# Optimization experiments

Measured on AMD Instinct MI355X. Metric: run time of the kernel, lower is better.

## Reference

```python
import jax, jax.numpy as jnp
import numpy as np

N_NODES = 50000
N_EDGES = 800000
EPS = 1e-5


def setup_inputs() -> dict:
    key = jax.random.key(0)
    ks = jax.random.split(key, 8)
    x = jax.random.normal(ks[0], (N_NODES, 4), dtype=jnp.float32)
    edge_index = jax.random.randint(ks[1], (2, N_EDGES), 0, N_NODES, dtype=jnp.int64)
    edge_attr = jax.random.normal(ks[2], (N_EDGES, 84), dtype=jnp.float32)
    # nnconv1 (acts as Linear(88,128) over concatenated per-edge features)
    W1 = jax.random.normal(ks[3], (88, 128), dtype=jnp.float32) * (1.0 / np.sqrt(88))
    b1 = jnp.zeros((128,), dtype=jnp.float32)
    # BatchNorm1d(128) affine params
    gamma = jnp.ones((128,), dtype=jnp.float32)
    beta = jnp.zeros((128,), dtype=jnp.float32)
    # node_mlp_2: Linear(132,64) + ReLU
    W2 = jax.random.normal(ks[4], (132, 64), dtype=jnp.float32) * (1.0 / np.sqrt(132))
    b2 = jnp.zeros((64,), dtype=jnp.float32)
    return {"x": x, "edge_index": edge_index, "edge_attr": edge_attr,
            "W1": W1, "b1": b1, "gamma": gamma, "beta": beta, "W2": W2, "b2": b2}


def reference(x, edge_index, edge_attr, W1, b1, gamma, beta, W2, b2):
    row, col = edge_index[0], edge_index[1]
    n_nodes = x.shape[0]
    # gather + concat: [E, 4+84=88]
    h = jnp.concatenate([x[col], edge_attr], axis=1)
    # edge-conditioned linear (NNConv wrapper == Linear(88,128)): [E,128]
    h = h @ W1 + b1
    # BatchNorm1d over edge batch dim (training mode, biased var as torch)
    mean = jnp.mean(h, axis=0)
    var = jnp.mean((h - mean) ** 2, axis=0)
    h = (h - mean) * jax.lax.rsqrt(var + EPS) * gamma + beta
    # scatter_mean over row -> [N,128]
    agg = jax.ops.segment_sum(h, row, num_segments=n_nodes)
    cnt = jax.ops.segment_sum(jnp.ones((h.shape[0],), dtype=h.dtype), row,
                              num_segments=n_nodes)
    agg = agg / jnp.clip(cnt, 1.0)[:, None]
    # concat + MLP: [N, 4+128=132] -> [N,64]
    out = jnp.concatenate([x, agg], axis=1)
    return jax.nn.relu(out @ W2 + b2)
```

## Files before the change

kernel.cpp:

```cpp
#include <hip/hip_runtime.h>
#include <hip/hip_bf16.h>

#define E_EDGES 800000
#define N_NODES_ 50000
#define EPS_ 1e-5f
#define N_SCAN_BLOCKS 49

#define M_GRID   625
#define M_ITERS  10
#define M_SPLITS 25

typedef float f32x4 __attribute__((ext_vector_type(4)));
typedef short s16x8 __attribute__((ext_vector_type(8)));

#define OFF_M      0
#define OFF_CS     (88 * 88)
#define OFF_CNT    (OFF_CS + 88)
#define ZERO_WORDS (OFF_CNT + N_NODES_)
#define OFF_AGG    ZERO_WORDS
#define OFF_CUR    (OFF_AGG + N_NODES_ * 88)
#define OFF_PART   (OFF_CUR + N_NODES_)
#define OFF_PERM   (OFF_PART + 64)
#define OFF_V      (OFF_PERM + E_EDGES)
#define OFF_S      (OFF_V + 88 * 128)
#define OFF_T      (OFF_S + 128)
#define OFF_MPART  (OFF_T + 128)

__global__ __launch_bounds__(256, 3)
void m_kernel(const float* __restrict__ x, const int* __restrict__ eidx,
              const float* __restrict__ ea, float* __restrict__ mpart)
{
    __shared__ __align__(16) short Gs_t[96 * 136];

    const int tid  = threadIdx.x;
    const int lane = tid & 63;
    const int wave = tid >> 6;
    const int m    = lane & 15;
    const int q    = lane >> 4;

    f32x4 acc[6];
#pragma unroll
    for (int i = 0; i < 6; ++i) acc[i] = (f32x4){0.f, 0.f, 0.f, 0.f};

    {
        int* gz = (int*)&Gs_t[88 * 136];
        for (int i = tid; i < 8 * 136 / 2; i += 256) gz[i] = 0;
    }

    unsigned addrL[21];
#pragma unroll
    for (int i = 0; i < 21; ++i) {
        const int d = (i * 256 + tid) * 2;
        const int e = d / 84;
        const int f = d - e * 84;
        addrL[i] = (unsigned)((4 + f) * 136 + e);
    }

    int tile = blockIdx.x;
    int colA = 0, colB = 0;
    if (tid < 128) colA = eidx[E_EDGES + tile * 128 + tid];
    float2 r[21];
    {
        const float2* tb = (const float2*)ea + (size_t)tile * 5376;
#pragma unroll
        for (int i = 0; i < 21; ++i) r[i] = tb[i * 256 + tid];
    }
    float4 xv = (float4){0.f, 0.f, 0.f, 0.f};
    if (tid < 128) xv = *(const float4*)(x + (size_t)colA * 4);
    if (tid < 128) colB = eidx[E_EDGES + (tile + M_GRID) * 128 + tid];

#pragma unroll 1
    for (int it = 0; it < M_ITERS; ++it) {
        __syncthreads();

        if (tid < 128) {
            __hip_bfloat16 b0 = __float2bfloat16(xv.x);
            __hip_bfloat16 b1 = __float2bfloat16(xv.y);
            __hip_bfloat16 b2 = __float2bfloat16(xv.z);
            __hip_bfloat16 b3 = __float2bfloat16(xv.w);
            Gs_t[0 * 136 + tid] = *(short*)&b0;
            Gs_t[1 * 136 + tid] = *(short*)&b1;
            Gs_t[2 * 136 + tid] = *(short*)&b2;
            Gs_t[3 * 136 + tid] = *(short*)&b3;
        }
#pragma unroll
        for (int i = 0; i < 21; ++i) {
            __hip_bfloat16 b0 = __float2bfloat16(r[i].x);
            __hip_bfloat16 b1 = __float2bfloat16(r[i].y);
            Gs_t[addrL[i]]       = *(short*)&b0;
            Gs_t[addrL[i] + 136] = *(short*)&b1;
        }

        const int next = tile + M_GRID;
        if (it + 1 < M_ITERS) {
            const float2* tbn = (const float2*)ea + (size_t)next * 5376;
#pragma unroll
            for (int i = 0; i < 21; ++i) r[i] = tbn[i * 256 + tid];
            if (tid < 128) xv = *(const float4*)(x + (size_t)colB * 4);
            if (tid < 128 && it + 2 < M_ITERS)
                colB = eidx[E_EDGES + (next + M_GRID) * 128 + tid];
        }
        __syncthreads();

#pragma unroll
        for (int kk = 0; kk < 4; ++kk) {
            const int kbase = kk * 32 + q * 8;
            s16x8 fr[6];
#pragma unroll
            for (int p = 0; p < 6; ++p)
                fr[p] = *reinterpret_cast<const s16x8*>(
                            &Gs_t[(p * 16 + m) * 136 + kbase]);
#define MM(i, a, b) acc[i] = __builtin_amdgcn_mfma_f32_16x16x32_bf16(fr[a], fr[b], acc[i], 0, 0, 0)
            if      (wave == 0) { MM(0,0,0); MM(1,0,4); MM(2,1,3); MM(3,2,3); MM(4,3,4); MM(5,5,5); }
            else if (wave == 1) { MM(0,0,1); MM(1,0,5); MM(2,1,4); MM(3,2,4); MM(4,3,5); }
            else if (wave == 2) { MM(0,0,2); MM(1,1,1); MM(2,1,5); MM(3,2,5); MM(4,4,4); }
            else                { MM(0,0,3); MM(1,1,2); MM(2,2,2); MM(3,3,3); MM(4,4,5); }
#undef MM
        }
        tile = next;
    }

    {
        float* pb = mpart + (size_t)blockIdx.x * 5376;
        const int nt = (wave == 0) ? 6 : 5;
#pragma unroll
        for (int i = 0; i < 6; ++i) {
            if (i < nt) {
                const int k = wave + i * 4;
                *(f32x4*)(pb + k * 256 + m * 16 + q * 4) = acc[i];
            }
        }
    }
}

__global__ __launch_bounds__(256)
void m_reduce_kernel(const float* __restrict__ mpart, float* __restrict__ M)
{
    const int g     = blockIdx.x * 256 + threadIdx.x;
    const int pos   = g % 5376;
    const int split = g / 5376;
    const int b0    = split * (M_GRID / M_SPLITS);
    const int b1    = b0 + (M_GRID / M_SPLITS);

    float s = 0.f;
#pragma unroll 5
    for (int b = b0; b < b1; ++b) s += mpart[(size_t)b * 5376 + pos];

    const int k  = pos >> 8;
    const int wi = pos & 255;
    const int m  = wi >> 4;
    const int qr = wi & 15;
    const int tr = (k >= 20) ? 5 : (k >= 18) ? 4 : (k >= 15) ? 3
                 : (k >= 11) ? 2 : (k >= 6) ? 1 : 0;
    const int S  = (tr == 5) ? 20 : (tr == 4) ? 18 : (tr == 3) ? 15
                 : (tr == 2) ? 11 : (tr == 1) ? 6 : 0;
    const int tc = tr + (k - S);
    const int rr = tr * 16 + qr;
    const int c  = tc * 16 + m;
    if (rr < 88 && c < 88) {
        atomicAdd(&M[rr * 88 + c], s);
        if (tr != tc) atomicAdd(&M[c * 88 + rr], s);
    }
}

__global__ void hist_kernel(const int* __restrict__ eidx, int* __restrict__ cnt)
{
    int e = blockIdx.x * 256 + threadIdx.x;
    if (e < E_EDGES) atomicAdd(&cnt[eidx[e]], 1);
}

__global__ void scan1_kernel(const int* __restrict__ cnt, int* __restrict__ partial)
{
    __shared__ int l[1024];
    int i = blockIdx.x * 1024 + threadIdx.x;
    l[threadIdx.x] = (i < N_NODES_) ? cnt[i] : 0;
    __syncthreads();
    for (int s = 512; s > 0; s >>= 1) {
        if (threadIdx.x < s) l[threadIdx.x] += l[threadIdx.x + s];
        __syncthreads();
    }
    if (threadIdx.x == 0) partial[blockIdx.x] = l[0];
}

__global__ void scan2_kernel(int* __restrict__ partial)
{
    if (threadIdx.x == 0) {
        int acc = 0;
        for (int i = 0; i < N_SCAN_BLOCKS; ++i) {
            int t = partial[i]; partial[i] = acc; acc += t;
        }
    }
}

__global__ void scan3_kernel(const int* __restrict__ cnt, const int* __restrict__ partial,
                             int* __restrict__ cursor)
{
    __shared__ int l[1024];
    int i = blockIdx.x * 1024 + threadIdx.x;
    int v = (i < N_NODES_) ? cnt[i] : 0;
    l[threadIdx.x] = v;
    __syncthreads();
    for (int s = 1; s < 1024; s <<= 1) {
        int t = (threadIdx.x >= s) ? l[threadIdx.x - s] : 0;
        __syncthreads();
        l[threadIdx.x] += t;
        __syncthreads();
    }
    if (i < N_NODES_) cursor[i] = partial[blockIdx.x] + l[threadIdx.x] - v;
}

__global__ void scatter_kernel(const int* __restrict__ eidx, int* __restrict__ cursor,
                               int* __restrict__ perm)
{
    int e = blockIdx.x * 256 + threadIdx.x;
    if (e < E_EDGES) {
        int pos = atomicAdd(&cursor[eidx[e]], 1);
        perm[pos] = e;
    }
}

__global__ __launch_bounds__(256)
void agg_kernel(const float* __restrict__ x, const int* __restrict__ eidx,
                const float* __restrict__ ea, const int* __restrict__ perm,
                const int* __restrict__ cursor, const int* __restrict__ cnt,
                float* __restrict__ agg)
{
    __shared__ float comb[2][88];
    const int tid  = threadIdx.x;
    const int w    = tid >> 6;
    const int lane = tid & 63;
    const int nloc = w >> 1;
    const int par  = w & 1;
    const int node = blockIdx.x * 2 + nloc;

    const int end = cursor[node];
    float a0 = 0.f, a1 = 0.f;
    int i = end - cnt[node] + par;
    if (i < end) {
        int e   = perm[i];
        int col = eidx[E_EDGES + e];
        for (; i < end; i += 2) {
            const float* p = ea + (size_t)e * 84;
            float v0 = (lane < 4) ? x[(size_t)col * 4 + lane] : p[lane - 4];
            float v1 = (lane < 24) ? p[60 + lane] : 0.f;
            int e_n = 0, col_n = 0;
            if (i + 2 < end) {
                e_n   = perm[i + 2];
                col_n = eidx[E_EDGES + e_n];
            }
            a0 += v0;
            a1 += v1;
            e = e_n; col = col_n;
        }
    }
    if (par == 1) {
        comb[nloc][lane] = a0;
        if (lane < 24) comb[nloc][64 + lane] = a1;
    }
    __syncthreads();
    if (par == 0) {
        a0 += comb[nloc][lane];
        if (lane < 24) a1 += comb[nloc][64 + lane];
        agg[(size_t)node * 88 + lane] = a0;
        if (lane < 24) agg[(size_t)node * 88 + 64 + lane] = a1;
    }
}

__global__ void colsum_kernel(const float* __restrict__ agg, float* __restrict__ cs)
{
    const int f = threadIdx.x;
    if (f >= 88) return;
    float a = 0.f;
    for (int n = blockIdx.x; n < N_NODES_; n += gridDim.x) a += agg[n * 88 + f];
    atomicAdd(&cs[f], a);
}

__global__ void mv_kernel(const float* __restrict__ M, const float* __restrict__ W1,
                          float* __restrict__ v)
{
    const int a = blockIdx.x;
    const int j = threadIdx.x;
    float acc = 0.f;
    for (int b = 0; b < 88; ++b) acc += M[a * 88 + b] * W1[b * 128 + j];
    v[a * 128 + j] = acc;
}

__global__ void stats_kernel(const float* __restrict__ cs, const float* __restrict__ v,
                             const float* __restrict__ W1, const float* __restrict__ b1,
                             const float* __restrict__ gamma, const float* __restrict__ beta,
                             float* __restrict__ s, float* __restrict__ t)
{
    const int j = threadIdx.x;
    const float invE = 1.0f / (float)E_EDGES;
    float mu = 0.f, eh2 = 0.f;
    for (int a = 0; a < 88; ++a) {
        float w = W1[a * 128 + j];
        mu  += cs[a] * w;
        eh2 += v[a * 128 + j] * w;
    }
    mu *= invE;
    eh2 *= invE;
    float var  = eh2 - mu * mu;
    float mean = mu + b1[j];
    float inv  = rsqrtf(var + EPS_);
    float sj   = gamma[j] * inv;
    s[j] = sj;
    t[j] = beta[j] - mean * sj;
}

__global__ __launch_bounds__(128)
void node_kernel(const float* __restrict__ x, const float* __restrict__ agg,
                 const int* __restrict__ cnt, const float* __restrict__ W1,
                 const float* __restrict__ b1, const float* __restrict__ W2,
                 const float* __restrict__ b2, const float* __restrict__ s,
                 const float* __restrict__ t, float* __restrict__ out)
{
    __shared__ float aggL[4 * 88];
    __shared__ float featL[4][128];
    __shared__ float cntL[4];
    __shared__ float xL[16];
    const int tid = threadIdx.x;
    const int nbase = blockIdx.x * 4;

    for (int i = tid; i < 352; i += 128) aggL[i] = agg[nbase * 88 + i];
    if (tid < 4)  cntL[tid] = (float)cnt[nbase + tid];
    if (tid < 16) xL[tid] = x[nbase * 4 + tid];
    __syncthreads();

    {
        const int j = tid;
        float a0 = 0.f, a1 = 0.f, a2 = 0.f, a3 = 0.f;
        for (int a = 0; a < 88; ++a) {
            float w = W1[a * 128 + j];
            a0 += aggL[a]       * w;
            a1 += aggL[88 + a]  * w;
            a2 += aggL[176 + a] * w;
            a3 += aggL[264 + a] * w;
        }
        const float sj = s[j], tj = t[j], bj = b1[j];
        float accs[4] = {a0, a1, a2, a3};
#pragma unroll
        for (int n = 0; n < 4; ++n) {
            float c = cntL[n];
            featL[n][j] = (c > 0.f) ? (sj * (accs[n] / c + bj) + tj) : 0.f;
        }
    }
    __syncthreads();

    {
        const int jc = tid & 63;
        const int nh = tid >> 6;
#pragma unroll
        for (int h = 0; h < 2; ++h) {
            const int n = nh * 2 + h;
            float acc = b2[jc];
#pragma unroll
            for (int k = 0; k < 4; ++k) acc += xL[n * 4 + k] * W2[k * 64 + jc];
            for (int k = 0; k < 128; ++k)
                acc += featL[n][k] * W2[(4 + k) * 64 + jc];
            out[(nbase + n) * 64 + jc] = fmaxf(acc, 0.f);
        }
    }
}

extern "C" void kernel_launch(void* const* d_in, const int* in_sizes, int n_in,
                              void* d_out, int out_size, void* d_ws, size_t ws_size,
                              hipStream_t stream)
{
    const float* x     = (const float*)d_in[0];
    const int*   eidx  = (const int*)d_in[1];
    const float* ea    = (const float*)d_in[2];
    const float* W1    = (const float*)d_in[3];
    const float* b1    = (const float*)d_in[4];
    const float* gamma = (const float*)d_in[5];
    const float* beta  = (const float*)d_in[6];
    const float* W2    = (const float*)d_in[7];
    const float* b2    = (const float*)d_in[8];

    float* ws    = (float*)d_ws;
    float* M     = ws + OFF_M;
    float* cs    = ws + OFF_CS;
    int*   cnt   = (int*)(ws + OFF_CNT);
    float* agg   = ws + OFF_AGG;
    int*   cur   = (int*)(ws + OFF_CUR);
    int*   part  = (int*)(ws + OFF_PART);
    int*   perm  = (int*)(ws + OFF_PERM);
    float* v     = ws + OFF_V;
    float* s     = ws + OFF_S;
    float* t     = ws + OFF_T;
    float* mpart = ws + OFF_MPART;
    float* out   = (float*)d_out;

    hipMemsetAsync(d_ws, 0, (size_t)ZERO_WORDS * sizeof(float), stream);

    hist_kernel<<<(E_EDGES + 255) / 256, 256, 0, stream>>>(eidx, cnt);
    scan1_kernel<<<N_SCAN_BLOCKS, 1024, 0, stream>>>(cnt, part);
    scan2_kernel<<<1, 64, 0, stream>>>(part);
    scan3_kernel<<<N_SCAN_BLOCKS, 1024, 0, stream>>>(cnt, part, cur);
    scatter_kernel<<<(E_EDGES + 255) / 256, 256, 0, stream>>>(eidx, cur, perm);

    m_kernel<<<M_GRID, 256, 0, stream>>>(x, eidx, ea, mpart);
    m_reduce_kernel<<<(5376 * M_SPLITS) / 256, 256, 0, stream>>>(mpart, M);
    agg_kernel<<<N_NODES_ / 2, 256, 0, stream>>>(x, eidx, ea, perm, cur, cnt, agg);

    colsum_kernel<<<512, 96, 0, stream>>>(agg, cs);
    mv_kernel<<<88, 128, 0, stream>>>(M, W1, v);
    stats_kernel<<<1, 128, 0, stream>>>(cs, v, W1, b1, gamma, beta, s, t);
    node_kernel<<<12500, 128, 0, stream>>>(x, agg, cnt, W1, b1, W2, b2, s, t, out);
}
```

Before: 758.7 us.

## Make agg_kernel edge-parallel with segmented atomics and double m_kernel grid

The aggregation kernel now gives each wave a fixed chunk of 16 sorted edges instead of one node. It accumulates runs of equal destination rows in registers and flushes each run to the node's aggregate with atomicAdd. This removes load imbalance from variable node degree and the serial per-node pointer chasing, at the cost of atomics and zeroing the agg buffer in the memset. Separately, m_kernel runs twice as many blocks with half the iterations each, and its launch-bounds occupancy hint rises from 3 to 6.

```diff
diff --git a/kernel.cpp b/kernel.cpp
--- a/kernel.cpp
+++ b/kernel.cpp
@@ -6,9 +6,11 @@
 #define EPS_ 1e-5f
 #define N_SCAN_BLOCKS 49
 
-#define M_GRID   625
-#define M_ITERS  10
+#define M_GRID   1250
+#define M_ITERS  5
 #define M_SPLITS 25
+
+#define AGG_EPW  16
 
 typedef float f32x4 __attribute__((ext_vector_type(4)));
 typedef short s16x8 __attribute__((ext_vector_type(8)));
@@ -16,9 +18,9 @@
 #define OFF_M      0
 #define OFF_CS     (88 * 88)
 #define OFF_CNT    (OFF_CS + 88)
-#define ZERO_WORDS (OFF_CNT + N_NODES_)
-#define OFF_AGG    ZERO_WORDS
-#define OFF_CUR    (OFF_AGG + N_NODES_ * 88)
+#define OFF_AGG    (OFF_CNT + N_NODES_)
+#define ZERO_WORDS (OFF_AGG + N_NODES_ * 88)
+#define OFF_CUR    ZERO_WORDS
 #define OFF_PART   (OFF_CUR + N_NODES_)
 #define OFF_PERM   (OFF_PART + 64)
 #define OFF_V      (OFF_PERM + E_EDGES)
@@ -26,7 +28,7 @@
 #define OFF_T      (OFF_S + 128)
 #define OFF_MPART  (OFF_T + 128)
 
-__global__ __launch_bounds__(256, 3)
+__global__ __launch_bounds__(256, 6)
 void m_kernel(const float* __restrict__ x, const int* __restrict__ eidx,
               const float* __restrict__ ea, float* __restrict__ mpart)
 {
@@ -222,48 +224,45 @@
 __global__ __launch_bounds__(256)
 void agg_kernel(const float* __restrict__ x, const int* __restrict__ eidx,
                 const float* __restrict__ ea, const int* __restrict__ perm,
-                const int* __restrict__ cursor, const int* __restrict__ cnt,
                 float* __restrict__ agg)
 {
-    __shared__ float comb[2][88];
+    __shared__ int eL[4][AGG_EPW];
+    __shared__ int rL[4][AGG_EPW];
+    __shared__ int cL[4][AGG_EPW];
+
     const int tid  = threadIdx.x;
-    const int w    = tid >> 6;
     const int lane = tid & 63;
-    const int nloc = w >> 1;
-    const int par  = w & 1;
-    const int node = blockIdx.x * 2 + nloc;
-
-    const int end = cursor[node];
+    const int wv   = tid >> 6;
+    const int base = (blockIdx.x * 4 + wv) * AGG_EPW;
+
+    if (lane < AGG_EPW) {
+        int e = perm[base + lane];
+        eL[wv][lane] = e;
+        rL[wv][lane] = eidx[e];
+        cL[wv][lane] = eidx[E_EDGES + e];
+    }
+    __syncthreads();
+
     float a0 = 0.f, a1 = 0.f;
-    int i = end - cnt[node] + par;
-    if (i < end) {
-        int e   = perm[i];
-        int col = eidx[E_EDGES + e];
-        for (; i < end; i += 2) {
-            const float* p = ea + (size_t)e * 84;
-            float v0 = (lane < 4) ? x[(size_t)col * 4 + lane] : p[lane - 4];
-            float v1 = (lane < 24) ? p[60 + lane] : 0.f;
-            int e_n = 0, col_n = 0;
-            if (i + 2 < end) {
-                e_n   = perm[i + 2];
-                col_n = eidx[E_EDGES + e_n];
-            }
-            a0 += v0;
-            a1 += v1;
-            e = e_n; col = col_n;
-        }
-    }
-    if (par == 1) {
-        comb[nloc][lane] = a0;
-        if (lane < 24) comb[nloc][64 + lane] = a1;
-    }
-    __syncthreads();
-    if (par == 0) {
-        a0 += comb[nloc][lane];
-        if (lane < 24) a1 += comb[nloc][64 + lane];
-        agg[(size_t)node * 88 + lane] = a0;
-        if (lane < 24) agg[(size_t)node * 88 + 64 + lane] = a1;
-    }
+    int cur = rL[wv][0];
+#pragma unroll
+    for (int j = 0; j < AGG_EPW; ++j) {
+        const int e   = eL[wv][j];
+        const int row = rL[wv][j];
+        const int col = cL[wv][j];
+        const float* p = ea + (size_t)e * 84;
+        float v0 = (lane < 4) ? x[(size_t)col * 4 + lane] : p[lane - 4];
+        float v1 = (lane < 24) ? p[60 + lane] : 0.f;
+        if (row != cur) {
+            atomicAdd(&agg[(size_t)cur * 88 + lane], a0);
+            if (lane < 24) atomicAdd(&agg[(size_t)cur * 88 + 64 + lane], a1);
+            a0 = 0.f; a1 = 0.f; cur = row;
+        }
+        a0 += v0;
+        a1 += v1;
+    }
+    atomicAdd(&agg[(size_t)cur * 88 + lane], a0);
+    if (lane < 24) atomicAdd(&agg[(size_t)cur * 88 + 64 + lane], a1);
 }
 
 __global__ void colsum_kernel(const float* __restrict__ agg, float* __restrict__ cs)
@@ -401,7 +400,7 @@
 
     m_kernel<<<M_GRID, 256, 0, stream>>>(x, eidx, ea, mpart);
     m_reduce_kernel<<<(5376 * M_SPLITS) / 256, 256, 0, stream>>>(mpart, M);
-    agg_kernel<<<N_NODES_ / 2, 256, 0, stream>>>(x, eidx, ea, perm, cur, cnt, agg);
+    agg_kernel<<<E_EDGES / (4 * AGG_EPW), 256, 0, stream>>>(x, eidx, ea, perm, agg);
 
     colsum_kernel<<<512, 96, 0, stream>>>(agg, cs);
     mv_kernel<<<88, 128, 0, stream>>>(M, W1, v);
```

New measurement: 837.6 us. 1.1x slower.
